# Kernel optimization log

Hardware: AMD Instinct MI355X
Metric: run time of the kernel (lower is better)

The kernel has to match this reference:

```python
import jax, jax.numpy as jnp
import numpy as np

N, D, OUT = 8192, 512, 1

def setup_inputs() -> dict:
    key = jax.random.key(0)
    ks = jax.random.split(key, 7)
    s2 = (2.0 / (D + OUT)) ** 0.5  # GlorotNormal-ish scale
    return {
        "x": jax.random.normal(ks[0], (N, D), jnp.float32),
        "mu_kernel": jax.random.normal(ks[1], (D, OUT), jnp.float32) * s2,
        "rho_kernel": jax.random.normal(ks[2], (D,), jnp.float32) * (2.0 / (D + 1)) ** 0.5,
        "var_kernel": jax.random.normal(ks[3], (D, OUT), jnp.float32) * s2,
        "mu_bias": jax.random.normal(ks[4], (OUT,), jnp.float32) * 0.1,
        "var_bias": jax.random.normal(ks[5], (OUT,), jnp.float32) * 0.1,
        "cov_bias": jax.random.normal(ks[6], (OUT,), jnp.float32) * 0.1,
    }

def reference(x, mu_kernel, rho_kernel, var_kernel, mu_bias, var_bias, cov_bias):
    # mean head: (n, out)
    mu = x @ mu_kernel + mu_bias
    # diagonal variances: softplus(x @ W_v + b_v) + eps, squeezed to (n,)
    d = jax.nn.softplus(x @ var_kernel + var_bias) + 1e-8
    d = jnp.squeeze(d, axis=-1)
    # off-diagonal covariances: sum_k x_i[k]*x_j[k]*rho[k] + cov_bias
    # == (x * rho_kernel) @ x.T  (fused GEMM; avoids the (n,n,d) tile)
    rho = (x * rho_kernel) @ x.T + cov_bias  # (n, n), cov_bias broadcasts (out=1)
    idx = jnp.arange(x.shape[0])
    cov = rho.at[idx, idx].set(d)  # tf.linalg.set_diag
    return (mu, cov)
```

## Files before the change

kernel.cpp:

```cpp
#include <hip/hip_runtime.h>
#include <hip/hip_bf16.h>
#include <math.h>

#define AS1 __attribute__((address_space(1)))
#define AS3 __attribute__((address_space(3)))

typedef _Float16 f16x8 __attribute__((ext_vector_type(8)));
typedef float f32x4 __attribute__((ext_vector_type(4)));

#define NROWS 8192
#define DDIM  512

__global__ __launch_bounds__(256) void prep_kernel(
    const float* __restrict__ x,
    const float* __restrict__ muk,
    const float* __restrict__ rho,
    const float* __restrict__ vark,
    const float* __restrict__ mu_bias,
    const float* __restrict__ var_bias,
    float* __restrict__ mu_out,
    _Float16* __restrict__ xh,
    _Float16* __restrict__ ah,
    float* __restrict__ dvec)
{
    const int wave = threadIdx.x >> 6;
    const int lane = threadIdx.x & 63;
    const int row  = blockIdx.x * 4 + wave;
    const int k    = lane * 8;

    const float4 x0 = *(const float4*)(x + (size_t)row * DDIM + k);
    const float4 x1 = *(const float4*)(x + (size_t)row * DDIM + k + 4);
    const float4 m0 = *(const float4*)(muk + k);
    const float4 m1 = *(const float4*)(muk + k + 4);
    const float4 r0 = *(const float4*)(rho + k);
    const float4 r1 = *(const float4*)(rho + k + 4);
    const float4 v0 = *(const float4*)(vark + k);
    const float4 v1 = *(const float4*)(vark + k + 4);

    float xv[8] = {x0.x, x0.y, x0.z, x0.w, x1.x, x1.y, x1.z, x1.w};
    float rv[8] = {r0.x, r0.y, r0.z, r0.w, r1.x, r1.y, r1.z, r1.w};
    float mv[8] = {m0.x, m0.y, m0.z, m0.w, m1.x, m1.y, m1.z, m1.w};
    float vv[8] = {v0.x, v0.y, v0.z, v0.w, v1.x, v1.y, v1.z, v1.w};

    f16x8 hx, ha;
    float dm = 0.f, dv = 0.f;
#pragma unroll
    for (int j = 0; j < 8; ++j) {
        hx[j] = (_Float16)xv[j];
        ha[j] = (_Float16)(xv[j] * rv[j]);
        dm += xv[j] * mv[j];
        dv += xv[j] * vv[j];
    }
    *(f16x8*)(xh + (size_t)row * DDIM + k) = hx;
    *(f16x8*)(ah + (size_t)row * DDIM + k) = ha;

#pragma unroll
    for (int off = 32; off > 0; off >>= 1) {
        dm += __shfl_down(dm, off, 64);
        dv += __shfl_down(dv, off, 64);
    }
    if (lane == 0) {
        mu_out[row] = dm + mu_bias[0];
        float z  = dv + var_bias[0];
        float sp = fmaxf(z, 0.f) + log1pf(expf(-fabsf(z)));
        dvec[row] = sp + 1e-8f;
    }
}

__device__ __forceinline__ void gload_lds16(const void* g, void* l)
{
    __builtin_amdgcn_global_load_lds((AS1 void*)g, (AS3 void*)l, 16, 0, 0);
}

__global__ __launch_bounds__(256) void cov_kernel(
    const _Float16* __restrict__ A,
    const _Float16* __restrict__ B,
    const float* __restrict__ dvec,
    const float* __restrict__ cov_bias,
    float* __restrict__ C)
{
    __shared__ _Float16 As[128 * 32];
    __shared__ _Float16 Bs[128 * 32];

    const int t    = threadIdx.x;
    const int lane = t & 63;
    const int wave = t >> 6;
    const int wr   = wave >> 1;
    const int wc   = wave & 1;
    const int quad = lane >> 4;
    const int l16  = lane & 15;

    const int tt = blockIdx.x;
    int bi = (int)((sqrtf(8.f * (float)tt + 1.f) - 1.f) * 0.5f);
    while ((bi + 1) * (bi + 2) / 2 <= tt) ++bi;
    while (bi * (bi + 1) / 2 > tt) --bi;
    const int bj = tt - bi * (bi + 1) / 2;

    const int rowBase = bi * 128;
    const int colBase = bj * 128;
    const float cb = cov_bias[0];

    f32x4 acc[4][4] = {};

    const _Float16* ga = A + ((size_t)(rowBase + (t >> 2))) * DDIM + (t & 3) * 8;
    const _Float16* gb = B + ((size_t)(colBase + (t >> 2))) * DDIM + (t & 3) * 8;

#pragma unroll 1
    for (int kt = 0; kt < 16; ++kt) {
        const int k0 = kt * 32;
        gload_lds16(ga + k0,             As + t * 8);
        gload_lds16(ga + 64 * DDIM + k0, As + 2048 + t * 8);
        gload_lds16(gb + k0,             Bs + t * 8);
        gload_lds16(gb + 64 * DDIM + k0, Bs + 2048 + t * 8);
        __syncthreads();

        f16x8 af[4], bf[4];
#pragma unroll
        for (int i = 0; i < 4; ++i)
            af[i] = *(const f16x8*)(As + (wr * 64 + i * 16 + l16) * 32 + quad * 8);
#pragma unroll
        for (int j = 0; j < 4; ++j)
            bf[j] = *(const f16x8*)(Bs + (wc * 64 + j * 16 + l16) * 32 + quad * 8);

#pragma unroll
        for (int i = 0; i < 4; ++i)
#pragma unroll
            for (int j = 0; j < 4; ++j)
                acc[i][j] = __builtin_amdgcn_mfma_f32_16x16x32_f16(af[i], bf[j], acc[i][j], 0, 0, 0);
        __syncthreads();
    }

#pragma unroll
    for (int i = 0; i < 4; ++i) {
        const int grb = rowBase + wr * 64 + i * 16 + quad * 4;
#pragma unroll
        for (int j = 0; j < 4; ++j) {
            const int gc = colBase + wc * 64 + j * 16 + l16;
#pragma unroll
            for (int r = 0; r < 4; ++r) {
                const int gr = grb + r;
                float v = acc[i][j][r] + cb;
                if (gr == gc) v = dvec[gr];
                C[(size_t)gr * NROWS + gc] = v;
            }
        }
    }

    if (bi != bj) {
#pragma unroll
        for (int j = 0; j < 4; ++j) {
            const int trow = colBase + wc * 64 + j * 16 + l16;
#pragma unroll
            for (int i = 0; i < 4; ++i) {
                const int tcol = rowBase + wr * 64 + i * 16 + quad * 4;
                float4 v;
                v.x = acc[i][j][0] + cb;
                v.y = acc[i][j][1] + cb;
                v.z = acc[i][j][2] + cb;
                v.w = acc[i][j][3] + cb;
                *(float4*)(C + (size_t)trow * NROWS + tcol) = v;
            }
        }
    }
}

extern "C" void kernel_launch(void* const* d_in, const int* in_sizes, int n_in,
                              void* d_out, int out_size, void* d_ws, size_t ws_size,
                              hipStream_t stream)
{
    const float* x     = (const float*)d_in[0];
    const float* muk   = (const float*)d_in[1];
    const float* rho   = (const float*)d_in[2];
    const float* vark  = (const float*)d_in[3];
    const float* mu_b  = (const float*)d_in[4];
    const float* var_b = (const float*)d_in[5];
    const float* cov_b = (const float*)d_in[6];

    float* out = (float*)d_out;

    _Float16* xh = (_Float16*)d_ws;
    _Float16* ah = xh + (size_t)NROWS * DDIM;
    float* dvec  = (float*)(ah + (size_t)NROWS * DDIM);

    prep_kernel<<<NROWS / 4, 256, 0, stream>>>(x, muk, rho, vark, mu_b, var_b,
                                               out, xh, ah, dvec);

    const int nblk = (NROWS / 128) * (NROWS / 128 + 1) / 2;
    cov_kernel<<<nblk, 256, 0, stream>>>(ah, xh, dvec, cov_b, out + NROWS);
}
```

Before: 360.7 us.

## Double-buffer LDS tiles, swizzle tile order, and vectorize epilogue stores via LDS

Adds a two-stage LDS buffer so the next K-slice is fetched while MFMAs run on the current one, and removes one barrier per iteration. Remaps block IDs so that adjacent workgroups spread across the triangular tile space. The direct-tile epilogue is transposed through per-wave LDS scratch so that each lane writes a float4 instead of scalar stores. The risks are extra LDS usage, and diagonal handling that now depends on an in-register patch.

Result: slower. 375.2 us (+4.0%).

```diff
diff --git a/kernel.cpp b/kernel.cpp
--- a/kernel.cpp
+++ b/kernel.cpp
@@ -1,5 +1,4 @@
 #include <hip/hip_runtime.h>
-#include <hip/hip_bf16.h>
 #include <math.h>
 
 #define AS1 __attribute__((address_space(1)))
@@ -79,8 +78,8 @@
     const float* __restrict__ cov_bias,
     float* __restrict__ C)
 {
-    __shared__ _Float16 As[128 * 32];
-    __shared__ _Float16 Bs[128 * 32];
+    __shared__ _Float16 As[2][128 * 32];
+    __shared__ _Float16 Bs[2][128 * 32];
 
     const int t    = threadIdx.x;
     const int lane = t & 63;
@@ -90,7 +89,9 @@
     const int quad = lane >> 4;
     const int l16  = lane & 15;
 
-    const int tt = blockIdx.x;
+    const int bid = blockIdx.x;
+    const int tt  = (bid & 7) * (2080 / 8) + (bid >> 3);
+
     int bi = (int)((sqrtf(8.f * (float)tt + 1.f) - 1.f) * 0.5f);
     while ((bi + 1) * (bi + 2) / 2 <= tt) ++bi;
     while (bi * (bi + 1) / 2 > tt) --bi;
@@ -105,44 +106,62 @@
     const _Float16* ga = A + ((size_t)(rowBase + (t >> 2))) * DDIM + (t & 3) * 8;
     const _Float16* gb = B + ((size_t)(colBase + (t >> 2))) * DDIM + (t & 3) * 8;
 
+    gload_lds16(ga,             As[0] + t * 8);
+    gload_lds16(ga + 64 * DDIM, As[0] + 2048 + t * 8);
+    gload_lds16(gb,             Bs[0] + t * 8);
+    gload_lds16(gb + 64 * DDIM, Bs[0] + 2048 + t * 8);
+    __syncthreads();
+
 #pragma unroll 1
     for (int kt = 0; kt < 16; ++kt) {
-        const int k0 = kt * 32;
-        gload_lds16(ga + k0,             As + t * 8);
-        gload_lds16(ga + 64 * DDIM + k0, As + 2048 + t * 8);
-        gload_lds16(gb + k0,             Bs + t * 8);
-        gload_lds16(gb + 64 * DDIM + k0, Bs + 2048 + t * 8);
-        __syncthreads();
+        const int cur = kt & 1;
+
+        if (kt < 15) {
+            const int k0 = (kt + 1) * 32;
+            gload_lds16(ga + k0,             As[cur ^ 1] + t * 8);
+            gload_lds16(ga + 64 * DDIM + k0, As[cur ^ 1] + 2048 + t * 8);
+            gload_lds16(gb + k0,             Bs[cur ^ 1] + t * 8);
+            gload_lds16(gb + 64 * DDIM + k0, Bs[cur ^ 1] + 2048 + t * 8);
+        }
 
         f16x8 af[4], bf[4];
 #pragma unroll
         for (int i = 0; i < 4; ++i)
-            af[i] = *(const f16x8*)(As + (wr * 64 + i * 16 + l16) * 32 + quad * 8);
+            af[i] = *(const f16x8*)(As[cur] + (wr * 64 + i * 16 + l16) * 32 + quad * 8);
 #pragma unroll
         for (int j = 0; j < 4; ++j)
-            bf[j] = *(const f16x8*)(Bs + (wc * 64 + j * 16 + l16) * 32 + quad * 8);
+            bf[j] = *(const f16x8*)(Bs[cur] + (wc * 64 + j * 16 + l16) * 32 + quad * 8);
 
 #pragma unroll
         for (int i = 0; i < 4; ++i)
 #pragma unroll
             for (int j = 0; j < 4; ++j)
                 acc[i][j] = __builtin_amdgcn_mfma_f32_16x16x32_f16(af[i], bf[j], acc[i][j], 0, 0, 0);
+
         __syncthreads();
     }
 
+    float* sc = (float*)(&As[0][0]) + wave * (16 * 20);
+
 #pragma unroll
     for (int i = 0; i < 4; ++i) {
-        const int grb = rowBase + wr * 64 + i * 16 + quad * 4;
+        const int grb = rowBase + wr * 64 + i * 16;
 #pragma unroll
         for (int j = 0; j < 4; ++j) {
-            const int gc = colBase + wc * 64 + j * 16 + l16;
-#pragma unroll
-            for (int r = 0; r < 4; ++r) {
-                const int gr = grb + r;
-                float v = acc[i][j][r] + cb;
-                if (gr == gc) v = dvec[gr];
-                C[(size_t)gr * NROWS + gc] = v;
+            const int gcb = colBase + wc * 64 + j * 16;
+#pragma unroll
+            for (int r = 0; r < 4; ++r)
+                sc[(quad * 4 + r) * 20 + l16] = acc[i][j][r] + cb;
+            asm volatile("s_waitcnt lgkmcnt(0)" ::: "memory");
+            float4 v = *(const float4*)(sc + l16 * 20 + quad * 4);
+
+            const int gr = grb + l16;
+            const int gc = gcb + quad * 4;
+            if (bi == bj) {
+                const int c = gr - gc;
+                if (0 <= c && c < 4) ((float*)&v)[c] = dvec[gr];
             }
+            *(float4*)(C + (size_t)gr * NROWS + gc) = v;
         }
     }
 
```

## Triple-buffer LDS K-loop with async prefetch, XOR swizzle, and block remap

Applied to the files above, without the earlier changes.

Turns the single-buffered GEMM K-loop into a three-stage LDS pipeline. Global-to-LDS loads for later k-tiles are issued while MFMAs run on the current tile, and explicit vmcnt waits and barriers replace the two __syncthreads per iteration. An XOR swizzle on the LDS column chunk is meant to cut bank conflicts, and block IDs are remapped with stride 8 across the triangle, likely to spread work across XCDs or improve cache locality. The epilogue is split so off-diagonal tiles skip the per-element diagonal check. In exchange the kernel uses three times the LDS, which may lower occupancy, and it relies on hand-tuned waitcnt values being correct.

New measurement: 346.9 us. 1.04x faster.

```diff
diff --git a/kernel.cpp b/kernel.cpp
--- a/kernel.cpp
+++ b/kernel.cpp
@@ -1,5 +1,4 @@
 #include <hip/hip_runtime.h>
-#include <hip/hip_bf16.h>
 #include <math.h>
 
 #define AS1 __attribute__((address_space(1)))
@@ -79,8 +78,8 @@
     const float* __restrict__ cov_bias,
     float* __restrict__ C)
 {
-    __shared__ _Float16 As[128 * 32];
-    __shared__ _Float16 Bs[128 * 32];
+    __shared__ _Float16 As[3][128 * 32];
+    __shared__ _Float16 Bs[3][128 * 32];
 
     const int t    = threadIdx.x;
     const int lane = t & 63;
@@ -89,8 +88,11 @@
     const int wc   = wave & 1;
     const int quad = lane >> 4;
     const int l16  = lane & 15;
-
-    const int tt = blockIdx.x;
+    const int xc   = quad ^ ((l16 >> 1) & 3);
+
+    const int bid = blockIdx.x;
+    const int tt  = (bid & 7) * (2080 / 8) + (bid >> 3);
+
     int bi = (int)((sqrtf(8.f * (float)tt + 1.f) - 1.f) * 0.5f);
     while ((bi + 1) * (bi + 2) / 2 <= tt) ++bi;
     while (bi * (bi + 1) / 2 > tt) --bi;
@@ -102,51 +104,103 @@
 
     f32x4 acc[4][4] = {};
 
-    const _Float16* ga = A + ((size_t)(rowBase + (t >> 2))) * DDIM + (t & 3) * 8;
-    const _Float16* gb = B + ((size_t)(colBase + (t >> 2))) * DDIM + (t & 3) * 8;
+    const int sr = t >> 2;
+    const int sg = (t & 3) ^ ((sr >> 1) & 3);
+    const _Float16* ga = A + ((size_t)(rowBase + sr)) * DDIM + sg * 8;
+    const _Float16* gb = B + ((size_t)(colBase + sr)) * DDIM + sg * 8;
+
+#define STAGE(kt, s) do {                                            \
+        const int _k0 = (kt) * 32;                                   \
+        gload_lds16(ga + _k0,             As[s] + t * 8);            \
+        gload_lds16(ga + 64 * DDIM + _k0, As[s] + 2048 + t * 8);     \
+        gload_lds16(gb + _k0,             Bs[s] + t * 8);            \
+        gload_lds16(gb + 64 * DDIM + _k0, Bs[s] + 2048 + t * 8);     \
+    } while (0)
+
+    f16x8 af[4], bf[4];
+
+#define DSREAD(s) do {                                                          \
+        _Pragma("unroll")                                                       \
+        for (int _i = 0; _i < 4; ++_i)                                          \
+            af[_i] = *(const f16x8*)(As[s] + (wr * 64 + _i * 16 + l16) * 32 + xc * 8); \
+        _Pragma("unroll")                                                       \
+        for (int _j = 0; _j < 4; ++_j)                                          \
+            bf[_j] = *(const f16x8*)(Bs[s] + (wc * 64 + _j * 16 + l16) * 32 + xc * 8); \
+    } while (0)
+
+#define DOMFMA() do {                                                           \
+        _Pragma("unroll")                                                       \
+        for (int _i = 0; _i < 4; ++_i)                                          \
+            _Pragma("unroll")                                                   \
+            for (int _j = 0; _j < 4; ++_j)                                      \
+                acc[_i][_j] = __builtin_amdgcn_mfma_f32_16x16x32_f16(           \
+                    af[_i], bf[_j], acc[_i][_j], 0, 0, 0);                      \
+    } while (0)
+
+    STAGE(0, 0);
+    STAGE(1, 1);
+    STAGE(2, 2);
+    asm volatile("s_waitcnt vmcnt(8)" ::: "memory");
+    __builtin_amdgcn_s_barrier();
 
 #pragma unroll 1
-    for (int kt = 0; kt < 16; ++kt) {
-        const int k0 = kt * 32;
-        gload_lds16(ga + k0,             As + t * 8);
-        gload_lds16(ga + 64 * DDIM + k0, As + 2048 + t * 8);
-        gload_lds16(gb + k0,             Bs + t * 8);
-        gload_lds16(gb + 64 * DDIM + k0, Bs + 2048 + t * 8);
-        __syncthreads();
-
-        f16x8 af[4], bf[4];
-#pragma unroll
-        for (int i = 0; i < 4; ++i)
-            af[i] = *(const f16x8*)(As + (wr * 64 + i * 16 + l16) * 32 + quad * 8);
-#pragma unroll
-        for (int j = 0; j < 4; ++j)
-            bf[j] = *(const f16x8*)(Bs + (wc * 64 + j * 16 + l16) * 32 + quad * 8);
-
-#pragma unroll
-        for (int i = 0; i < 4; ++i)
-#pragma unroll
-            for (int j = 0; j < 4; ++j)
-                acc[i][j] = __builtin_amdgcn_mfma_f32_16x16x32_f16(af[i], bf[j], acc[i][j], 0, 0, 0);
-        __syncthreads();
-    }
-
-#pragma unroll
-    for (int i = 0; i < 4; ++i) {
-        const int grb = rowBase + wr * 64 + i * 16 + quad * 4;
-#pragma unroll
-        for (int j = 0; j < 4; ++j) {
-            const int gc = colBase + wc * 64 + j * 16 + l16;
-#pragma unroll
-            for (int r = 0; r < 4; ++r) {
-                const int gr = grb + r;
-                float v = acc[i][j][r] + cb;
-                if (gr == gc) v = dvec[gr];
-                C[(size_t)gr * NROWS + gc] = v;
+    for (int kt = 0; kt < 13; ++kt) {
+        const int s = kt % 3;
+        DSREAD(s);
+        asm volatile("s_waitcnt lgkmcnt(0)" ::: "memory");
+        __builtin_amdgcn_s_barrier();
+        STAGE(kt + 3, s);
+        DOMFMA();
+        asm volatile("s_waitcnt vmcnt(8)" ::: "memory");
+        __builtin_amdgcn_s_barrier();
+    }
+
+    DSREAD(1);
+    DOMFMA();
+    asm volatile("s_waitcnt vmcnt(4)" ::: "memory");
+    __builtin_amdgcn_s_barrier();
+
+    DSREAD(2);
+    DOMFMA();
+    asm volatile("s_waitcnt vmcnt(0)" ::: "memory");
+    __builtin_amdgcn_s_barrier();
+
+    DSREAD(0);
+    DOMFMA();
+
+#undef STAGE
+#undef DSREAD
+#undef DOMFMA
+
+    if (bi == bj) {
+#pragma unroll
+        for (int i = 0; i < 4; ++i) {
+            const int grb = rowBase + wr * 64 + i * 16 + quad * 4;
+#pragma unroll
+            for (int j = 0; j < 4; ++j) {
+                const int gc = colBase + wc * 64 + j * 16 + l16;
+#pragma unroll
+                for (int r = 0; r < 4; ++r) {
+                    const int gr = grb + r;
+                    float v = acc[i][j][r] + cb;
+                    if (gr == gc) v = dvec[gr];
+                    C[(size_t)gr * NROWS + gc] = v;
+                }
             }
         }
-    }
-
-    if (bi != bj) {
+    } else {
+#pragma unroll
+        for (int i = 0; i < 4; ++i) {
+            const int grb = rowBase + wr * 64 + i * 16 + quad * 4;
+#pragma unroll
+            for (int j = 0; j < 4; ++j) {
+                const int gc = colBase + wc * 64 + j * 16 + l16;
+#pragma unroll
+                for (int r = 0; r < 4; ++r)
+                    C[(size_t)(grb + r) * NROWS + gc] = acc[i][j][r] + cb;
+            }
+        }
+
 #pragma unroll
         for (int j = 0; j < 4; ++j) {
             const int trow = colBase + wc * 64 + j * 16 + l16;
```
